# Kernel tuning notes

Measured on AMD Instinct MI355X. Metric: run time of the kernel, lower is better.

## Reference

```python
import jax, jax.numpy as jnp
import numpy as np

NUM_NODES = 100000
NUM_HYPEREDGES = 20000
NUM_SEMALINKS = 5000
NUM_EDGES = 600000
IN_DIM = 128
SIGNAL_DIM = 64
OUT_DIM = 128


def setup_inputs() -> dict:
    key = jax.random.key(0)
    k = jax.random.split(key, 8)
    node_embeddings = jax.random.normal(k[0], (NUM_NODES, IN_DIM), dtype=jnp.float32)
    semalink_embeddings = jax.random.normal(k[1], (NUM_SEMALINKS, SIGNAL_DIM), dtype=jnp.float32)
    hyperedge_embeddings = jax.random.normal(k[2], (NUM_HYPEREDGES, IN_DIM), dtype=jnp.float32)
    node_idx = jax.random.randint(k[3], (NUM_EDGES,), 0, NUM_NODES, dtype=jnp.int32)
    sl_idx = jax.random.randint(k[4], (NUM_EDGES,), 0, NUM_SEMALINKS, dtype=jnp.int32)
    he_idx = jax.random.randint(k[5], (NUM_EDGES,), 0, NUM_HYPEREDGES, dtype=jnp.int32)
    semalinks = jnp.stack([node_idx, sl_idx, he_idx], axis=1)  # [E, 3]
    W_a = jax.random.normal(k[6], (IN_DIM, SIGNAL_DIM), dtype=jnp.float32)
    W_f = jax.random.normal(k[7], (2 * IN_DIM, OUT_DIM), dtype=jnp.float32)
    return {
        'node_embeddings': node_embeddings,
        'semalink_embeddings': semalink_embeddings,
        'hyperedge_embeddings': hyperedge_embeddings,
        'semalinks': semalinks,
        'W_a': W_a,
        'W_f': W_f,
    }


def reference(node_embeddings, semalink_embeddings, hyperedge_embeddings, semalinks, W_a, W_f):
    # Original loops edges in order, ASSIGNING final_embeddings[node_idx] each time:
    # only the LAST edge touching each node determines that node's output.
    E = semalinks.shape[0]
    n_idx = semalinks[:, 0]
    s_idx = semalinks[:, 1]
    h_idx = semalinks[:, 2]

    order = jnp.arange(E, dtype=jnp.int32)
    last = jax.ops.segment_max(order, n_idx, num_segments=NUM_NODES)  # [N]
    has_edge = last >= 0
    last_c = jnp.clip(last, 0, E - 1)

    sel_h = h_idx[last_c]  # [N]
    sel_s = s_idx[last_c]  # [N]
    h_emb = hyperedge_embeddings[sel_h]          # [N, in_dim]
    sl_emb = semalink_embeddings[sel_s]          # [N, signal_dim]

    # per-node attention score (1x1 in original)
    r_h = node_embeddings @ W_a                  # [N, signal_dim]
    r_t = h_emb @ W_a                            # [N, signal_dim]
    score = jnp.sum(r_h * jnp.tanh(r_t + sl_emb), axis=-1, keepdims=True)  # [N, 1]
    gamma = jax.nn.softmax(score, axis=-1)       # softmax over singleton == 1.0 (same as torch)
    f = gamma * h_emb                            # [N, in_dim]

    u = jnp.concatenate([f, node_embeddings], axis=-1) @ W_f  # [N, out_dim]
    out = jnp.where(has_edge[:, None], u, jnp.zeros((), dtype=u.dtype))
    return out
```

## Files before the change

kernel.cpp:

```cpp
#include <hip/hip_runtime.h>
#include <hip/hip_bf16.h>

#define NNODES 100000
#define NHE 20000
#define NEDGES 600000

typedef float f32x4 __attribute__((ext_vector_type(4)));
typedef short bf16x8 __attribute__((ext_vector_type(8)));
typedef short bf16x4 __attribute__((ext_vector_type(4)));
typedef int i32x4 __attribute__((ext_vector_type(4)));
typedef unsigned long long u64;

__device__ __forceinline__ unsigned short f2bf(float f) {
    unsigned u = __builtin_bit_cast(unsigned, f);
    u += 0x7fffu + ((u >> 16) & 1u);
    return (unsigned short)(u >> 16);
}
__device__ __forceinline__ float bf2f(unsigned short h) {
    unsigned u = ((unsigned)h) << 16;
    return __builtin_bit_cast(float, u);
}

__global__ void k0(u64* __restrict__ packed, const float* __restrict__ Wf,
                   unsigned short* __restrict__ wt) {
    int b = blockIdx.x, t = threadIdx.x;
    if (b < 196) {
        int i = b * 256 + t;
        if (i < NNODES / 2) ((f32x4*)packed)[i] = (f32x4){0.f, 0.f, 0.f, 0.f};
    } else {
        int idx = (b - 196) * 256 + t;
        int k = idx >> 7, c = idx & 127;
        wt[c * 256 + k] = f2bf(Wf[idx]);
    }
}

__global__ __launch_bounds__(256) void k1(
    const int* __restrict__ sl, u64* __restrict__ packed,
    const float* __restrict__ he_emb, const unsigned short* __restrict__ wt,
    unsigned short* __restrict__ heo)
{
    int b = blockIdx.x, t = threadIdx.x;
    if (b < 586) {
        int tg = b * 256 + t;
        if (tg < NEDGES / 4) {
            const i32x4* s4 = (const i32x4*)sl;
            i32x4 a = s4[3 * tg], bb = s4[3 * tg + 1], c = s4[3 * tg + 2];
            int e0 = 4 * tg;
            atomicMax(&packed[a[0]], ((u64)(e0 + 1) << 32) | (unsigned)a[2]);
            atomicMax(&packed[a[3]], ((u64)(e0 + 2) << 32) | (unsigned)bb[1]);
            atomicMax(&packed[bb[2]], ((u64)(e0 + 3) << 32) | (unsigned)c[0]);
            atomicMax(&packed[c[1]], ((u64)(e0 + 4) << 32) | (unsigned)c[3]);
        }
        return;
    }

    __shared__ __align__(16) unsigned short Xs[64 * 128];
    int r0 = (b - 586) * 64;

    #pragma unroll
    for (int i = 0; i < 8; ++i) {
        int idx = i * 256 + t;
        int row = idx >> 5, q = idx & 31;
        int ri = r0 + row; if (ri >= NHE) ri = NHE - 1;
        f32x4 v = *(const f32x4*)(he_emb + (long)ri * 128 + q * 4);
        bf16x4 p;
        p[0] = (short)f2bf(v[0]); p[1] = (short)f2bf(v[1]);
        p[2] = (short)f2bf(v[2]); p[3] = (short)f2bf(v[3]);
        int byte = (row * 256 + q * 8) ^ ((row & 7) << 4);
        *(bf16x4*)((char*)Xs + byte) = p;
    }
    __syncthreads();

    int lane = t & 63, w = t >> 6;
    int wm = w >> 1, wn = w & 1;
    int l15 = lane & 15, l4 = lane >> 4;

    f32x4 acc[2][4] = {};
    #pragma unroll
    for (int kc = 0; kc < 2; ++kc)
        #pragma unroll
        for (int ks = 0; ks < 2; ++ks) {
            bf16x8 a[2], bb[4];
            #pragma unroll
            for (int fm = 0; fm < 2; ++fm) {
                int row = wm * 32 + fm * 16 + l15;
                int byte = (row * 256 + kc * 128 + ks * 64 + l4 * 16) ^ ((row & 7) << 4);
                a[fm] = *(const bf16x8*)((const char*)Xs + byte);
            }
            #pragma unroll
            for (int fn = 0; fn < 4; ++fn) {
                int col = wn * 64 + fn * 16 + l15;
                bb[fn] = *(const bf16x8*)(wt + (long)col * 256 + kc * 64 + ks * 32 + l4 * 8);
            }
            #pragma unroll
            for (int fm = 0; fm < 2; ++fm)
                #pragma unroll
                for (int fn = 0; fn < 4; ++fn)
                    acc[fm][fn] = __builtin_amdgcn_mfma_f32_16x16x32_bf16(
                        bb[fn], a[fm], acc[fm][fn], 0, 0, 0);
        }

    #pragma unroll
    for (int fm = 0; fm < 2; ++fm) {
        int ri = r0 + wm * 32 + fm * 16 + l15;
        if (ri < NHE) {
            #pragma unroll
            for (int fn = 0; fn < 4; ++fn) {
                bf16x4 p;
                p[0] = (short)f2bf(acc[fm][fn][0]);
                p[1] = (short)f2bf(acc[fm][fn][1]);
                p[2] = (short)f2bf(acc[fm][fn][2]);
                p[3] = (short)f2bf(acc[fm][fn][3]);
                *(bf16x4*)(heo + (long)ri * 128 + wn * 64 + fn * 16 + l4 * 4) = p;
            }
        }
    }
}

__global__ __launch_bounds__(256) void k_main(
    const float* __restrict__ node_emb,
    const u64* __restrict__ packed,
    const unsigned short* __restrict__ wt,
    const unsigned short* __restrict__ heo,
    float* __restrict__ out)
{
    __shared__ __align__(16) unsigned short Xs[2][64 * 128];

    int t = threadIdx.x;
    int lane = t & 63, w = t >> 6;
    int wm = w >> 1, wn = w & 1;
    int l15 = lane & 15, l4 = lane >> 4;

    bf16x8 B[4][4];
    #pragma unroll
    for (int kk = 0; kk < 4; ++kk)
        #pragma unroll
        for (int fn = 0; fn < 4; ++fn) {
            int col = wn * 64 + fn * 16 + l15;
            B[kk][fn] = *(const bf16x8*)(wt + (long)col * 256 + 128 + kk * 32 + l4 * 8);
        }

    int r0 = blockIdx.x * 64;
    int r1 = (blockIdx.x + 782) * 64;

    u64 p = 0;
    {
        int prow = r0 + wm * 32 + (lane & 31);
        if (lane < 32 && prow < NNODES) p = packed[prow];
    }
    f32x4 nv[8];
    #pragma unroll
    for (int i = 0; i < 8; ++i) {
        int idx = i * 256 + t;
        int row = idx >> 5, q = idx & 31;
        int ri = r0 + row; if (ri >= NNODES) ri = NNODES - 1;
        nv[i] = *(const f32x4*)(node_emb + (long)ri * 128 + q * 4);
    }

    #pragma unroll
    for (int j = 0; j < 2; ++j) {
        int rb = j ? r1 : r0;

        int he16 = (int)(p & 0xffffffffull);
        int v16 = (p != 0) ? 1 : 0;
        int hrow[2], vv[2];
        hrow[0] = __shfl(he16, l15, 64);       vv[0] = __shfl(v16, l15, 64);
        hrow[1] = __shfl(he16, 16 + l15, 64);  vv[1] = __shfl(v16, 16 + l15, 64);
        bf16x4 hv[2][4];
        #pragma unroll
        for (int fm = 0; fm < 2; ++fm)
            #pragma unroll
            for (int fn = 0; fn < 4; ++fn)
                hv[fm][fn] = *(const bf16x4*)(heo + (long)hrow[fm] * 128 +
                                              wn * 64 + fn * 16 + l4 * 4);

        #pragma unroll
        for (int i = 0; i < 8; ++i) {
            int idx = i * 256 + t;
            int row = idx >> 5, q = idx & 31;
            bf16x4 pk;
            pk[0] = (short)f2bf(nv[i][0]); pk[1] = (short)f2bf(nv[i][1]);
            pk[2] = (short)f2bf(nv[i][2]); pk[3] = (short)f2bf(nv[i][3]);
            int byte = (row * 256 + q * 8) ^ ((row & 7) << 4);
            *(bf16x4*)((char*)Xs[j] + byte) = pk;
        }

        if (j == 0) {
            p = 0;
            int prow = r1 + wm * 32 + (lane & 31);
            if (lane < 32 && prow < NNODES) p = packed[prow];
            #pragma unroll
            for (int i = 0; i < 8; ++i) {
                int idx = i * 256 + t;
                int row = idx >> 5, q = idx & 31;
                int ri = r1 + row; if (ri >= NNODES) ri = NNODES - 1;
                nv[i] = *(const f32x4*)(node_emb + (long)ri * 128 + q * 4);
            }
        }

        asm volatile("s_waitcnt lgkmcnt(0)" ::: "memory");
        __builtin_amdgcn_sched_barrier(0);
        __builtin_amdgcn_s_barrier();
        __builtin_amdgcn_sched_barrier(0);

        f32x4 acc[2][4] = {};
        #pragma unroll
        for (int kk = 0; kk < 4; ++kk) {
            bf16x8 a[2];
            #pragma unroll
            for (int fm = 0; fm < 2; ++fm) {
                int row = wm * 32 + fm * 16 + l15;
                int byte = (row * 256 + kk * 64 + l4 * 16) ^ ((row & 7) << 4);
                a[fm] = *(const bf16x8*)((const char*)Xs[j] + byte);
            }
            #pragma unroll
            for (int fm = 0; fm < 2; ++fm)
                #pragma unroll
                for (int fn = 0; fn < 4; ++fn)
                    acc[fm][fn] = __builtin_amdgcn_mfma_f32_16x16x32_bf16(
                        B[kk][fn], a[fm], acc[fm][fn], 0, 0, 0);
        }

        #pragma unroll
        for (int fm = 0; fm < 2; ++fm) {
            int ri = rb + wm * 32 + fm * 16 + l15;
            if (ri < NNODES) {
                int v = vv[fm];
                #pragma unroll
                for (int fn = 0; fn < 4; ++fn) {
                    f32x4 o;
                    #pragma unroll
                    for (int jj = 0; jj < 4; ++jj)
                        o[jj] = v ? (acc[fm][fn][jj] + bf2f((unsigned short)hv[fm][fn][jj]))
                                  : 0.0f;
                    *(f32x4*)(out + (long)ri * 128 + wn * 64 + fn * 16 + l4 * 4) = o;
                }
            }
        }
    }
}

extern "C" void kernel_launch(void* const* d_in, const int* in_sizes, int n_in,
                              void* d_out, int out_size, void* d_ws, size_t ws_size,
                              hipStream_t stream) {
    const float* node_emb = (const float*)d_in[0];
    const float* he_emb = (const float*)d_in[2];
    const int* sl = (const int*)d_in[3];
    const float* Wf = (const float*)d_in[5];
    float* out = (float*)d_out;

    u64* packed = (u64*)d_ws;
    unsigned short* wt = (unsigned short*)((char*)d_ws + 800000);
    unsigned short* heo = (unsigned short*)((char*)d_ws + 865536);

    k0<<<324, 256, 0, stream>>>(packed, Wf, wt);
    k1<<<586 + 313, 256, 0, stream>>>(sl, packed, he_emb, wt, heo);
    k_main<<<782, 256, 0, stream>>>(node_emb, packed, wt, heo, out);
}
```

Baseline: 69.95 us.

## Process two hyperedge tiles per block with prefetch and hoisted weight fragments

The hyperedge projection part of k1 now has each block handle two 64-row tiles instead of one, which halves those blocks from 313 to 157. Weight fragments are loaded into registers once per block and reused for both tiles. The second tile's global loads are issued before the first tile's MFMA work, into a double-buffered LDS array. This amortizes weight loads and hides memory latency, at the cost of more registers and fewer blocks for parallelism.

```diff
diff --git a/kernel.cpp b/kernel.cpp
--- a/kernel.cpp
+++ b/kernel.cpp
@@ -54,64 +54,94 @@
         return;
     }
 
-    __shared__ __align__(16) unsigned short Xs[64 * 128];
-    int r0 = (b - 586) * 64;
-
+    __shared__ __align__(16) unsigned short Xs[2][64 * 128];
+    int bb_ = b - 586;
+    int lane = t & 63, w = t >> 6;
+    int wm = w >> 1, wn = w & 1;
+    int l15 = lane & 15, l4 = lane >> 4;
+
+    bf16x8 B[4][4];
+    #pragma unroll
+    for (int kk = 0; kk < 4; ++kk)
+        #pragma unroll
+        for (int fn = 0; fn < 4; ++fn) {
+            int col = wn * 64 + fn * 16 + l15;
+            B[kk][fn] = *(const bf16x8*)(wt + (long)col * 256 + kk * 32 + l4 * 8);
+        }
+
+    int r0 = bb_ * 64;
+    int r1 = (bb_ + 157) * 64;
+
+    f32x4 nv[8];
     #pragma unroll
     for (int i = 0; i < 8; ++i) {
         int idx = i * 256 + t;
         int row = idx >> 5, q = idx & 31;
         int ri = r0 + row; if (ri >= NHE) ri = NHE - 1;
-        f32x4 v = *(const f32x4*)(he_emb + (long)ri * 128 + q * 4);
-        bf16x4 p;
-        p[0] = (short)f2bf(v[0]); p[1] = (short)f2bf(v[1]);
-        p[2] = (short)f2bf(v[2]); p[3] = (short)f2bf(v[3]);
-        int byte = (row * 256 + q * 8) ^ ((row & 7) << 4);
-        *(bf16x4*)((char*)Xs + byte) = p;
-    }
-    __syncthreads();
-
-    int lane = t & 63, w = t >> 6;
-    int wm = w >> 1, wn = w & 1;
-    int l15 = lane & 15, l4 = lane >> 4;
-
-    f32x4 acc[2][4] = {};
-    #pragma unroll
-    for (int kc = 0; kc < 2; ++kc)
-        #pragma unroll
-        for (int ks = 0; ks < 2; ++ks) {
-            bf16x8 a[2], bb[4];
+        nv[i] = *(const f32x4*)(he_emb + (long)ri * 128 + q * 4);
+    }
+
+    #pragma unroll
+    for (int j = 0; j < 2; ++j) {
+        int rb = j ? r1 : r0;
+
+        #pragma unroll
+        for (int i = 0; i < 8; ++i) {
+            int idx = i * 256 + t;
+            int row = idx >> 5, q = idx & 31;
+            bf16x4 pk;
+            pk[0] = (short)f2bf(nv[i][0]); pk[1] = (short)f2bf(nv[i][1]);
+            pk[2] = (short)f2bf(nv[i][2]); pk[3] = (short)f2bf(nv[i][3]);
+            int byte = (row * 256 + q * 8) ^ ((row & 7) << 4);
+            *(bf16x4*)((char*)Xs[j] + byte) = pk;
+        }
+
+        if (j == 0) {
+            #pragma unroll
+            for (int i = 0; i < 8; ++i) {
+                int idx = i * 256 + t;
+                int row = idx >> 5, q = idx & 31;
+                int ri = r1 + row; if (ri >= NHE) ri = NHE - 1;
+                nv[i] = *(const f32x4*)(he_emb + (long)ri * 128 + q * 4);
+            }
+        }
+
+        asm volatile("s_waitcnt lgkmcnt(0)" ::: "memory");
+        __builtin_amdgcn_sched_barrier(0);
+        __builtin_amdgcn_s_barrier();
+        __builtin_amdgcn_sched_barrier(0);
+
+        f32x4 acc[2][4] = {};
+        #pragma unroll
+        for (int kk = 0; kk < 4; ++kk) {
+            bf16x8 a[2];
             #pragma unroll
             for (int fm = 0; fm < 2; ++fm) {
                 int row = wm * 32 + fm * 16 + l15;
-                int byte = (row * 256 + kc * 128 + ks * 64 + l4 * 16) ^ ((row & 7) << 4);
-                a[fm] = *(const bf16x8*)((const char*)Xs + byte);
-            }
-            #pragma unroll
-            for (int fn = 0; fn < 4; ++fn) {
-                int col = wn * 64 + fn * 16 + l15;
-                bb[fn] = *(const bf16x8*)(wt + (long)col * 256 + kc * 64 + ks * 32 + l4 * 8);
+                int byte = (row * 256 + kk * 64 + l4 * 16) ^ ((row & 7) << 4);
+                a[fm] = *(const bf16x8*)((const char*)Xs[j] + byte);
             }
             #pragma unroll
             for (int fm = 0; fm < 2; ++fm)
                 #pragma unroll
                 for (int fn = 0; fn < 4; ++fn)
                     acc[fm][fn] = __builtin_amdgcn_mfma_f32_16x16x32_bf16(
-                        bb[fn], a[fm], acc[fm][fn], 0, 0, 0);
-        }
-
-    #pragma unroll
-    for (int fm = 0; fm < 2; ++fm) {
-        int ri = r0 + wm * 32 + fm * 16 + l15;
-        if (ri < NHE) {
-            #pragma unroll
-            for (int fn = 0; fn < 4; ++fn) {
-                bf16x4 p;
-                p[0] = (short)f2bf(acc[fm][fn][0]);
-                p[1] = (short)f2bf(acc[fm][fn][1]);
-                p[2] = (short)f2bf(acc[fm][fn][2]);
-                p[3] = (short)f2bf(acc[fm][fn][3]);
-                *(bf16x4*)(heo + (long)ri * 128 + wn * 64 + fn * 16 + l4 * 4) = p;
+                        B[kk][fn], a[fm], acc[fm][fn], 0, 0, 0);
+        }
+
+        #pragma unroll
+        for (int fm = 0; fm < 2; ++fm) {
+            int ri = rb + wm * 32 + fm * 16 + l15;
+            if (ri < NHE) {
+                #pragma unroll
+                for (int fn = 0; fn < 4; ++fn) {
+                    bf16x4 p;
+                    p[0] = (short)f2bf(acc[fm][fn][0]);
+                    p[1] = (short)f2bf(acc[fm][fn][1]);
+                    p[2] = (short)f2bf(acc[fm][fn][2]);
+                    p[3] = (short)f2bf(acc[fm][fn][3]);
+                    *(bf16x4*)(heo + (long)ri * 128 + wn * 64 + fn * 16 + l4 * 4) = p;
+                }
             }
         }
     }
@@ -254,6 +284,6 @@
     unsigned short* heo = (unsigned short*)((char*)d_ws + 865536);
 
     k0<<<324, 256, 0, stream>>>(packed, Wf, wt);
-    k1<<<586 + 313, 256, 0, stream>>>(sl, packed, he_emb, wt, heo);
+    k1<<<586 + 157, 256, 0, stream>>>(sl, packed, he_emb, wt, heo);
     k_main<<<782, 256, 0, stream>>>(node_emb, packed, wt, heo, out);
 }
```

After: 68.28 us, median of 2. -2.4%, faster.
